# Performance work log

Hardware: AMD Instinct MI355X
Metric: run time of the kernel (lower is better)

The kernel has to match this reference:

```python
import jax, jax.numpy as jnp
import numpy as np

N = 100000   # nodes
E = 625000   # edges
D = 128      # input feature dim
H = 128      # hidden_channels
L = 2        # num_layers
NEG = 0.2    # leaky relu negative slope
BN_EPS = 1e-5


def setup_inputs() -> dict:
    key = jax.random.key(0)
    ks = jax.random.split(key, 12)
    s = 0.05
    return {
        "x": jax.random.normal(ks[0], (N, D), jnp.float32),
        "edge_index": jax.random.randint(ks[1], (2, E), 0, N, dtype=jnp.int32),
        "Wl": jax.random.normal(ks[2], (L, D, H), jnp.float32) * s,   # GATv2 lin_l (source)
        "bl": jax.random.normal(ks[3], (L, H), jnp.float32) * s,
        "Wr": jax.random.normal(ks[4], (L, D, H), jnp.float32) * s,   # GATv2 lin_r (target)
        "br": jax.random.normal(ks[5], (L, H), jnp.float32) * s,
        "att": jax.random.normal(ks[6], (L, H), jnp.float32) * s,     # attention vector a
        "cb": jax.random.normal(ks[7], (L, H), jnp.float32) * s,      # conv output bias
        "Wlin": jax.random.normal(ks[8], (L, H, H), jnp.float32) * s, # extra Linear
        "blin": jax.random.normal(ks[9], (L, H), jnp.float32) * s,
        "gamma": jnp.ones((L, H), jnp.float32),                       # BatchNorm weight
        "beta": jnp.zeros((L, H), jnp.float32),                       # BatchNorm bias
    }


def reference(x, edge_index, Wl, bl, Wr, br, att, cb, Wlin, blin, gamma, beta):
    src, dst = edge_index[0], edge_index[1]
    for i in range(L):
        # GATv2Conv (1 head, no self-loops)
        xs = x @ Wl[i] + bl[i]                 # [N, H] source transform
        xd = x @ Wr[i] + br[i]                 # [N, H] target transform
        e = jax.nn.leaky_relu(xs[src] + xd[dst], NEG)   # [E, H]
        logits = e @ att[i]                    # [E]
        m = jax.ops.segment_max(logits, dst, num_segments=N)
        a = jnp.exp(logits - m[dst])
        denom = jax.ops.segment_sum(a, dst, num_segments=N) + 1e-16
        alpha = a / denom[dst]                 # scatter-softmax over dst
        out = jax.ops.segment_sum(alpha[:, None] * xs[src], dst, num_segments=N) + cb[i]
        # x += lin(x)
        out = out + out @ Wlin[i] + blin[i]
        # BatchNorm1d (training mode: batch stats, biased var)
        mu = out.mean(axis=0)
        var = out.var(axis=0)
        x = (out - mu) * jax.lax.rsqrt(var + BN_EPS) * gamma[i] + beta[i]
        if i < L - 1:
            x = jax.nn.relu(x)
    return x
```

## Files before the change

### kernel.cpp

```cpp
#include <hip/hip_runtime.h>

#define NN 100000
#define NE 625000
#define HD 128

typedef unsigned int u32;
typedef unsigned short u16;
typedef __bf16 bf16x8 __attribute__((ext_vector_type(8)));
typedef float f32x4 __attribute__((ext_vector_type(4)));

__device__ __forceinline__ u16 f2b(float f) {
  u32 u = __float_as_uint(f);
  u32 r = (u + 0x7FFFu + ((u >> 16) & 1u)) >> 16;
  return (u16)r;
}
__device__ __forceinline__ float b2f(u32 u) { return __uint_as_float(u << 16); }

__global__ void k_prep_w(const float* __restrict__ Wl, const float* __restrict__ Wr,
                         const float* __restrict__ Wlin, u16* __restrict__ Wt) {
  int i = blockIdx.x * blockDim.x + threadIdx.x;
  if (i >= 6 * 16384) return;
  int mat = i >> 14;
  int l = mat / 3, which = mat % 3;
  int rem = i & 16383;
  int hh = rem >> 7, dd = rem & 127;
  const float* src = (which == 0) ? Wl : (which == 1) ? Wr : Wlin;
  float v = src[l * 16384 + dd * 128 + hh];
  if (which == 2 && dd == hh) v += 1.0f;
  Wt[l * (3 * 16384) + which * 16384 + hh * 128 + dd] = f2b(v);
}

__global__ void k_cast_x(const float* __restrict__ x, u16* __restrict__ xb) {
  int i = blockIdx.x * blockDim.x + threadIdx.x;
  if (i >= NN * 32) return;
  float4 v = *(const float4*)(x + i * 4);
  uint2 o;
  o.x = (u32)f2b(v.x) | ((u32)f2b(v.y) << 16);
  o.y = (u32)f2b(v.z) | ((u32)f2b(v.w) << 16);
  *(uint2*)(xb + i * 4) = o;
}

__global__ void k_hist(const int* __restrict__ dst, int* __restrict__ deg) {
  int e = blockIdx.x * blockDim.x + threadIdx.x;
  if (e < NE) atomicAdd(&deg[dst[e]], 1);
}

__global__ void k_alloc(const int* __restrict__ deg, int* __restrict__ row_start,
                        int* __restrict__ cursor) {
  int idx = blockIdx.x * blockDim.x + threadIdx.x;
  int lane = threadIdx.x & 63;
  int v = (idx < NN) ? deg[idx] : 0;
  int incl = v;
  #pragma unroll
  for (int off = 1; off < 64; off <<= 1) {
    int t = __shfl_up(incl, off, 64);
    if (lane >= off) incl += t;
  }
  int total = __shfl(incl, 63, 64);
  int base = 0;
  if (lane == 63) base = atomicAdd(cursor, total);
  base = __shfl(base, 63, 64);
  if (idx < NN) row_start[idx] = base + incl - v;
}

__global__ void k_fill(const int* __restrict__ src, const int* __restrict__ dst,
                       const int* __restrict__ row_start, int* __restrict__ cnt,
                       int* __restrict__ ss) {
  int e = blockIdx.x * blockDim.x + threadIdx.x;
  if (e >= NE) return;
  int d = dst[e];
  int p = row_start[d] + atomicAdd(&cnt[d], 1);
  ss[p] = src[e];
}

__global__ __launch_bounds__(256) void k_gemm_big(
    const u16* __restrict__ A, const u16* __restrict__ Bt0, const u16* __restrict__ Bt1,
    const float* __restrict__ bias0, const float* __restrict__ bias1,
    u16* __restrict__ o0, u16* __restrict__ o1,
    const float* __restrict__ bn_sum, const float* __restrict__ bn_sq,
    const float* __restrict__ bn_g, const float* __restrict__ bn_b,
    float* __restrict__ st_sum, float* __restrict__ st_sq, int nB) {
  __shared__ __align__(16) u16 lA[128 * 132];
  __shared__ __align__(16) u16 lB[128 * 128];
  const int tid = threadIdx.x;
  const int m0 = blockIdx.x * 128;
  const int rr = tid >> 4;
  const int seg = tid & 15;
  const int sK = seg >> 2;
  const int qd = seg & 3;

  float mu[8], sc[8], bb[8];
  if (bn_sum) {
    const float invn = 1.0f / 100000.0f;
    #pragma unroll
    for (int j = 0; j < 8; ++j) {
      int c = seg * 8 + j;
      float m = bn_sum[c] * invn;
      float v = fmaxf(bn_sq[c] * invn - m * m, 0.f);
      mu[j] = m;
      sc[j] = rsqrtf(v + 1e-5f) * bn_g[c];
      bb[j] = bn_b[c];
    }
  }
  #pragma unroll
  for (int p = 0; p < 8; ++p) {
    int g = m0 + p * 16 + rr;
    int gc = (g < NN) ? g : (NN - 1);
    uint4 v = *(const uint4*)(A + gc * HD + seg * 8);
    if (bn_sum) {
      u32 w[4] = {v.x, v.y, v.z, v.w};
      #pragma unroll
      for (int k = 0; k < 4; ++k) {
        float lo = fmaxf((b2f(w[k] & 0xFFFFu) - mu[2 * k]) * sc[2 * k] + bb[2 * k], 0.f);
        float hi = fmaxf((b2f(w[k] >> 16) - mu[2 * k + 1]) * sc[2 * k + 1] + bb[2 * k + 1], 0.f);
        w[k] = (u32)f2b(lo) | ((u32)f2b(hi) << 16);
      }
      v.x = w[0]; v.y = w[1]; v.z = w[2]; v.w = w[3];
    }
    *(uint4*)(lA + ((p * 4 + sK) * 64 + qd * 16 + rr) * 8) = v;
  }
  #pragma unroll
  for (int p = 0; p < 8; ++p) {
    int n = p * 16 + rr;
    uint4 v = *(const uint4*)(Bt0 + n * HD + seg * 8);
    *(uint4*)(lB + ((p * 4 + sK) * 64 + qd * 16 + rr) * 8) = v;
  }
  __syncthreads();

  const int wv = tid >> 6;
  const int lane = tid & 63;
  const int colt = lane & 15;
  const int rq = (lane >> 4) * 4;
  bf16x8 af[2][4];
  #pragma unroll
  for (int tile = 0; tile < 2; ++tile)
    #pragma unroll
    for (int s = 0; s < 4; ++s)
      af[tile][s] = *(const bf16x8*)(lA + (((wv * 2 + tile) * 4 + s) * 64 + lane) * 8);
  __syncthreads();

  for (int pass = 0; pass < nB; ++pass) {
    if (pass == 1) {
      __syncthreads();
      #pragma unroll
      for (int p = 0; p < 8; ++p) {
        int n = p * 16 + rr;
        uint4 v = *(const uint4*)(Bt1 + n * HD + seg * 8);
        *(uint4*)(lB + ((p * 4 + sK) * 64 + qd * 16 + rr) * 8) = v;
      }
      __syncthreads();
    }
    u16* o = (pass == 0) ? o0 : o1;
    const float* bias = (pass == 0) ? bias0 : bias1;
    #pragma unroll
    for (int t = 0; t < 8; ++t) {
      bf16x8 bf[4];
      #pragma unroll
      for (int s = 0; s < 4; ++s)
        bf[s] = *(const bf16x8*)(lB + ((t * 4 + s) * 64 + lane) * 8);
      const int c = t * 16 + colt;
      const float bs = bias[c];
      #pragma unroll
      for (int tile = 0; tile < 2; ++tile) {
        f32x4 acc = {0.f, 0.f, 0.f, 0.f};
        #pragma unroll
        for (int s = 0; s < 4; ++s)
          acc = __builtin_amdgcn_mfma_f32_16x16x32_bf16(af[tile][s], bf[s], acc, 0, 0, 0);
        #pragma unroll
        for (int r = 0; r < 4; ++r) {
          int lrow = (wv * 2 + tile) * 16 + rq + r;
          lA[lrow * 132 + c] = f2b(acc[r] + bs);
        }
      }
    }
    __syncthreads();
    float s8[8], q8[8];
    #pragma unroll
    for (int j = 0; j < 8; ++j) { s8[j] = 0.f; q8[j] = 0.f; }
    const int q = tid >> 4;
    #pragma unroll
    for (int i = 0; i < 8; ++i) {
      int row = i * 16 + q;
      int g = m0 + row;
      if (g < NN) {
        uint4 v = *(const uint4*)(lA + row * 132 + seg * 8);
        *(uint4*)(o + g * HD + seg * 8) = v;
        if (st_sum && pass == 0) {
          u32 w[4] = {v.x, v.y, v.z, v.w};
          #pragma unroll
          for (int k = 0; k < 4; ++k) {
            float lo = b2f(w[k] & 0xFFFFu), hi = b2f(w[k] >> 16);
            s8[2 * k] += lo; q8[2 * k] += lo * lo;
            s8[2 * k + 1] += hi; q8[2 * k + 1] += hi * hi;
          }
        }
      }
    }
    if (st_sum && pass == 0) {
      __syncthreads();
      float* red = (float*)lB;
      #pragma unroll
      for (int j = 0; j < 8; ++j) {
        red[q * 128 + seg * 8 + j] = s8[j];
        red[2048 + q * 128 + seg * 8 + j] = q8[j];
      }
      __syncthreads();
      if (tid < 128) {
        float S = 0.f, Q = 0.f;
        #pragma unroll
        for (int u = 0; u < 16; ++u) {
          S += red[u * 128 + tid];
          Q += red[2048 + u * 128 + tid];
        }
        atomicAdd(&st_sum[tid], S);
        atomicAdd(&st_sq[tid], Q);
      }
    }
  }
}

__global__ __launch_bounds__(256) void k_edge2(
    const u16* __restrict__ xs_b, const u16* __restrict__ xd_b,
    const int* __restrict__ row_start, const int* __restrict__ deg,
    const int* __restrict__ ss, const float* __restrict__ att,
    const float* __restrict__ cb, u16* __restrict__ out_b) {
  int dv = blockIdx.x * 4 + (threadIdx.x >> 6);
  if (dv >= NN) return;
  int lane = threadIdx.x & 63;
  float a0 = att[2 * lane], a1 = att[2 * lane + 1];
  const u32* xs32 = (const u32*)xs_b;
  u32 xdp = ((const u32*)xd_b)[dv * 64 + lane];
  float xd0 = b2f(xdp & 0xFFFFu), xd1 = b2f(xdp >> 16);
  int base = row_start[dv], n = deg[dv];
  float acc0 = 0.f, acc1 = 0.f, wsum = 0.f;
  int e = 0;
  for (; e + 4 <= n; e += 4) {
    int s0 = ss[base + e], s1 = ss[base + e + 1];
    int s2 = ss[base + e + 2], s3 = ss[base + e + 3];
    u32 p0 = xs32[s0 * 64 + lane];
    u32 p1 = xs32[s1 * 64 + lane];
    u32 p2 = xs32[s2 * 64 + lane];
    u32 p3 = xs32[s3 * 64 + lane];
    float x00 = b2f(p0 & 0xFFFFu), x01 = b2f(p0 >> 16);
    float x10 = b2f(p1 & 0xFFFFu), x11 = b2f(p1 >> 16);
    float x20 = b2f(p2 & 0xFFFFu), x21 = b2f(p2 >> 16);
    float x30 = b2f(p3 & 0xFFFFu), x31 = b2f(p3 >> 16);
    float t;
    float q0, q1, q2, q3;
    t = x00 + xd0; q0  = a0 * (fmaxf(t, 0.f) + 0.2f * fminf(t, 0.f));
    t = x01 + xd1; q0 += a1 * (fmaxf(t, 0.f) + 0.2f * fminf(t, 0.f));
    t = x10 + xd0; q1  = a0 * (fmaxf(t, 0.f) + 0.2f * fminf(t, 0.f));
    t = x11 + xd1; q1 += a1 * (fmaxf(t, 0.f) + 0.2f * fminf(t, 0.f));
    t = x20 + xd0; q2  = a0 * (fmaxf(t, 0.f) + 0.2f * fminf(t, 0.f));
    t = x21 + xd1; q2 += a1 * (fmaxf(t, 0.f) + 0.2f * fminf(t, 0.f));
    t = x30 + xd0; q3  = a0 * (fmaxf(t, 0.f) + 0.2f * fminf(t, 0.f));
    t = x31 + xd1; q3 += a1 * (fmaxf(t, 0.f) + 0.2f * fminf(t, 0.f));
    #pragma unroll
    for (int off = 1; off < 64; off <<= 1) {
      q0 += __shfl_xor(q0, off, 64);
      q1 += __shfl_xor(q1, off, 64);
      q2 += __shfl_xor(q2, off, 64);
      q3 += __shfl_xor(q3, off, 64);
    }
    float w0 = __expf(q0), w1 = __expf(q1), w2 = __expf(q2), w3 = __expf(q3);
    wsum += (w0 + w1) + (w2 + w3);
    acc0 += w0 * x00 + w1 * x10 + w2 * x20 + w3 * x30;
    acc1 += w0 * x01 + w1 * x11 + w2 * x21 + w3 * x31;
  }
  for (; e < n; ++e) {
    int s = ss[base + e];
    u32 p = xs32[s * 64 + lane];
    float x0 = b2f(p & 0xFFFFu), x1 = b2f(p >> 16);
    float t0 = x0 + xd0, t1 = x1 + xd1;
    float q = a0 * (fmaxf(t0, 0.f) + 0.2f * fminf(t0, 0.f)) +
              a1 * (fmaxf(t1, 0.f) + 0.2f * fminf(t1, 0.f));
    #pragma unroll
    for (int off = 1; off < 64; off <<= 1) q += __shfl_xor(q, off, 64);
    float w = __expf(q);
    wsum += w; acc0 += w * x0; acc1 += w * x1;
  }
  float inv = 1.f / (wsum + 1e-16f);
  float o0 = acc0 * inv + cb[2 * lane];
  float o1 = acc1 * inv + cb[2 * lane + 1];
  ((u32*)out_b)[dv * 64 + lane] = (u32)f2b(o0) | ((u32)f2b(o1) << 16);
}

__global__ void k_bn(const u16* __restrict__ hb, const float* __restrict__ ssum,
                     const float* __restrict__ ssq, const float* __restrict__ gamma,
                     const float* __restrict__ beta, float* __restrict__ fout) {
  int i = blockIdx.x * blockDim.x + threadIdx.x;
  if (i >= NN * 64) return;
  int cp = (i & 63) * 2;
  u32 xp = ((const u32*)hb)[i];
  float v0 = b2f(xp & 0xFFFFu), v1 = b2f(xp >> 16);
  const float invn = 1.0f / 100000.0f;
  float mu0 = ssum[cp] * invn, mu1 = ssum[cp + 1] * invn;
  float va0 = fmaxf(ssq[cp] * invn - mu0 * mu0, 0.f);
  float va1 = fmaxf(ssq[cp + 1] * invn - mu1 * mu1, 0.f);
  float s0 = rsqrtf(va0 + 1e-5f) * gamma[cp];
  float s1 = rsqrtf(va1 + 1e-5f) * gamma[cp + 1];
  float o0 = (v0 - mu0) * s0 + beta[cp];
  float o1 = (v1 - mu1) * s1 + beta[cp + 1];
  int row = i >> 6;
  *(float2*)(fout + row * 128 + cp) = make_float2(o0, o1);
}

extern "C" void kernel_launch(void* const* d_in, const int* in_sizes, int n_in,
                              void* d_out, int out_size, void* d_ws, size_t ws_size,
                              hipStream_t stream) {
  const float* x    = (const float*)d_in[0];
  const int*   ei   = (const int*)d_in[1];
  const float* Wl   = (const float*)d_in[2];
  const float* bl   = (const float*)d_in[3];
  const float* Wr   = (const float*)d_in[4];
  const float* br   = (const float*)d_in[5];
  const float* att  = (const float*)d_in[6];
  const float* cb   = (const float*)d_in[7];
  const float* Wlin = (const float*)d_in[8];
  const float* blin = (const float*)d_in[9];
  const float* gm   = (const float*)d_in[10];
  const float* bt   = (const float*)d_in[11];
  const int* esrc = ei;
  const int* edst = ei + NE;

  u16* xb    = (u16*)d_ws;
  u16* xs_b  = xb + NN * HD;
  u16* xd_b  = xs_b + NN * HD;
  u16* out_b = xd_b + NN * HD;
  u16* Wt    = out_b + NN * HD;
  int* deg       = (int*)(Wt + 6 * 16384);
  int* cnt       = deg + NN;
  int* cursor    = cnt + NN;
  int* row_start = cursor + 1;
  int* srcs      = row_start + NN;
  float* ssum0   = (float*)(srcs + NE);
  float* ssq0    = ssum0 + 128;
  float* ssum1   = ssq0 + 128;
  float* ssq1    = ssum1 + 128;

  hipMemsetAsync(deg, 0, (size_t)(2 * NN + 1) * 4, stream);
  hipMemsetAsync(ssum0, 0, 4 * 128 * 4, stream);
  k_prep_w<<<(6 * 16384 + 255) / 256, 256, 0, stream>>>(Wl, Wr, Wlin, Wt);
  k_cast_x<<<(NN * 32 + 255) / 256, 256, 0, stream>>>(x, xb);
  k_hist<<<(NE + 255) / 256, 256, 0, stream>>>(edst, deg);
  k_alloc<<<(NN + 255) / 256, 256, 0, stream>>>(deg, row_start, cursor);
  k_fill<<<(NE + 255) / 256, 256, 0, stream>>>(esrc, edst, row_start, cnt, srcs);

  const int gg = (NN + 127) / 128;
  const u16* wt0_l = Wt;             const u16* wt0_r = Wt + 16384;     const u16* wt0_lin = Wt + 2 * 16384;
  const u16* wt1_l = Wt + 3 * 16384; const u16* wt1_r = Wt + 4 * 16384; const u16* wt1_lin = Wt + 5 * 16384;

  k_gemm_big<<<gg, 256, 0, stream>>>(xb, wt0_l, wt0_r, bl, br, xs_b, xd_b,
                                     nullptr, nullptr, nullptr, nullptr,
                                     nullptr, nullptr, 2);
  k_edge2<<<(NN + 3) / 4, 256, 0, stream>>>(xs_b, xd_b, row_start, deg, srcs,
                                            att, cb, out_b);
  k_gemm_big<<<gg, 256, 0, stream>>>(out_b, wt0_lin, nullptr, blin, nullptr,
                                     out_b, nullptr,
                                     nullptr, nullptr, nullptr, nullptr,
                                     ssum0, ssq0, 1);
  k_gemm_big<<<gg, 256, 0, stream>>>(out_b, wt1_l, wt1_r, bl + 128, br + 128,
                                     xs_b, xd_b,
                                     ssum0, ssq0, gm, bt,
                                     nullptr, nullptr, 2);
  k_edge2<<<(NN + 3) / 4, 256, 0, stream>>>(xs_b, xd_b, row_start, deg, srcs,
                                            att + 128, cb + 128, out_b);
  k_gemm_big<<<gg, 256, 0, stream>>>(out_b, wt1_lin, nullptr, blin + 128, nullptr,
                                     out_b, nullptr,
                                     nullptr, nullptr, nullptr, nullptr,
                                     ssum1, ssq1, 1);
  k_bn<<<(NN * 64 + 255) / 256, 256, 0, stream>>>(out_b, ssum1, ssq1,
                                                  gm + 128, bt + 128, (float*)d_out);
}
```

Measured before the change: 484.3 us.

## Load GEMM weights from global memory and batch edge-logit reductions across four edges

The GEMM kernel no longer stages the weight matrix in LDS. Each lane reads its bf16x8 B fragments straight from global/L2, which halves shared memory per block and removes one staging phase and its barriers. The edge kernel now computes leaky ReLU as 0.6*t+0.4*|t| on packed float2. It folds four edge logits into one shared butterfly reduction (transpose-style combining at offsets 1 and 2, then a single chain) instead of four full chains, and handles the tail with masked weights rather than a scalar remainder loop. The risks are repeated global weight reads per block and wasted lanes on low-degree nodes.

```diff
diff --git a/kernel.cpp b/kernel.cpp
--- a/kernel.cpp
+++ b/kernel.cpp
@@ -8,6 +8,7 @@
 typedef unsigned short u16;
 typedef __bf16 bf16x8 __attribute__((ext_vector_type(8)));
 typedef float f32x4 __attribute__((ext_vector_type(4)));
+typedef float f32x2 __attribute__((ext_vector_type(2)));
 
 __device__ __forceinline__ u16 f2b(float f) {
   u32 u = __float_as_uint(f);
@@ -73,7 +74,7 @@
   ss[p] = src[e];
 }
 
-__global__ __launch_bounds__(256) void k_gemm_big(
+__global__ __launch_bounds__(256) void k_gemm3(
     const u16* __restrict__ A, const u16* __restrict__ Bt0, const u16* __restrict__ Bt1,
     const float* __restrict__ bias0, const float* __restrict__ bias1,
     u16* __restrict__ o0, u16* __restrict__ o1,
@@ -81,7 +82,6 @@
     const float* __restrict__ bn_g, const float* __restrict__ bn_b,
     float* __restrict__ st_sum, float* __restrict__ st_sq, int nB) {
   __shared__ __align__(16) u16 lA[128 * 132];
-  __shared__ __align__(16) u16 lB[128 * 128];
   const int tid = threadIdx.x;
   const int m0 = blockIdx.x * 128;
   const int rr = tid >> 4;
@@ -119,18 +119,13 @@
     }
     *(uint4*)(lA + ((p * 4 + sK) * 64 + qd * 16 + rr) * 8) = v;
   }
-  #pragma unroll
-  for (int p = 0; p < 8; ++p) {
-    int n = p * 16 + rr;
-    uint4 v = *(const uint4*)(Bt0 + n * HD + seg * 8);
-    *(uint4*)(lB + ((p * 4 + sK) * 64 + qd * 16 + rr) * 8) = v;
-  }
   __syncthreads();
 
   const int wv = tid >> 6;
   const int lane = tid & 63;
   const int colt = lane & 15;
-  const int rq = (lane >> 4) * 4;
+  const int rq4 = lane >> 4;
+  const int rq = rq4 * 4;
   bf16x8 af[2][4];
   #pragma unroll
   for (int tile = 0; tile < 2; ++tile)
@@ -140,16 +135,8 @@
   __syncthreads();
 
   for (int pass = 0; pass < nB; ++pass) {
-    if (pass == 1) {
-      __syncthreads();
-      #pragma unroll
-      for (int p = 0; p < 8; ++p) {
-        int n = p * 16 + rr;
-        uint4 v = *(const uint4*)(Bt1 + n * HD + seg * 8);
-        *(uint4*)(lB + ((p * 4 + sK) * 64 + qd * 16 + rr) * 8) = v;
-      }
-      __syncthreads();
-    }
+    if (pass == 1) __syncthreads();
+    const u16* Bt = (pass == 0) ? Bt0 : Bt1;
     u16* o = (pass == 0) ? o0 : o1;
     const float* bias = (pass == 0) ? bias0 : bias1;
     #pragma unroll
@@ -157,7 +144,7 @@
       bf16x8 bf[4];
       #pragma unroll
       for (int s = 0; s < 4; ++s)
-        bf[s] = *(const bf16x8*)(lB + ((t * 4 + s) * 64 + lane) * 8);
+        bf[s] = *(const bf16x8*)(Bt + (t * 16 + colt) * HD + s * 32 + rq4 * 8);
       const int c = t * 16 + colt;
       const float bs = bias[c];
       #pragma unroll
@@ -198,7 +185,7 @@
     }
     if (st_sum && pass == 0) {
       __syncthreads();
-      float* red = (float*)lB;
+      float* red = (float*)lA;
       #pragma unroll
       for (int j = 0; j < 8; ++j) {
         red[q * 128 + seg * 8 + j] = s8[j];
@@ -219,7 +206,7 @@
   }
 }
 
-__global__ __launch_bounds__(256) void k_edge2(
+__global__ __launch_bounds__(256) void k_edge3(
     const u16* __restrict__ xs_b, const u16* __restrict__ xd_b,
     const int* __restrict__ row_start, const int* __restrict__ deg,
     const int* __restrict__ ss, const float* __restrict__ att,
@@ -227,61 +214,68 @@
   int dv = blockIdx.x * 4 + (threadIdx.x >> 6);
   if (dv >= NN) return;
   int lane = threadIdx.x & 63;
-  float a0 = att[2 * lane], a1 = att[2 * lane + 1];
+  float2 av = *(const float2*)(att + 2 * lane);
+  f32x2 a6 = {0.6f * av.x, 0.6f * av.y};
+  f32x2 a4 = {0.4f * av.x, 0.4f * av.y};
+  u32 xdp = ((const u32*)xd_b)[dv * 64 + lane];
+  f32x2 xd2 = {b2f(xdp & 0xFFFFu), b2f(xdp >> 16)};
+  int base = row_start[dv], n = deg[dv];
   const u32* xs32 = (const u32*)xs_b;
-  u32 xdp = ((const u32*)xd_b)[dv * 64 + lane];
-  float xd0 = b2f(xdp & 0xFFFFu), xd1 = b2f(xdp >> 16);
-  int base = row_start[dv], n = deg[dv];
-  float acc0 = 0.f, acc1 = 0.f, wsum = 0.f;
-  int e = 0;
-  for (; e + 4 <= n; e += 4) {
-    int s0 = ss[base + e], s1 = ss[base + e + 1];
-    int s2 = ss[base + e + 2], s3 = ss[base + e + 3];
-    u32 p0 = xs32[s0 * 64 + lane];
-    u32 p1 = xs32[s1 * 64 + lane];
-    u32 p2 = xs32[s2 * 64 + lane];
-    u32 p3 = xs32[s3 * 64 + lane];
-    float x00 = b2f(p0 & 0xFFFFu), x01 = b2f(p0 >> 16);
-    float x10 = b2f(p1 & 0xFFFFu), x11 = b2f(p1 >> 16);
-    float x20 = b2f(p2 & 0xFFFFu), x21 = b2f(p2 >> 16);
-    float x30 = b2f(p3 & 0xFFFFu), x31 = b2f(p3 >> 16);
-    float t;
-    float q0, q1, q2, q3;
-    t = x00 + xd0; q0  = a0 * (fmaxf(t, 0.f) + 0.2f * fminf(t, 0.f));
-    t = x01 + xd1; q0 += a1 * (fmaxf(t, 0.f) + 0.2f * fminf(t, 0.f));
-    t = x10 + xd0; q1  = a0 * (fmaxf(t, 0.f) + 0.2f * fminf(t, 0.f));
-    t = x11 + xd1; q1 += a1 * (fmaxf(t, 0.f) + 0.2f * fminf(t, 0.f));
-    t = x20 + xd0; q2  = a0 * (fmaxf(t, 0.f) + 0.2f * fminf(t, 0.f));
-    t = x21 + xd1; q2 += a1 * (fmaxf(t, 0.f) + 0.2f * fminf(t, 0.f));
-    t = x30 + xd0; q3  = a0 * (fmaxf(t, 0.f) + 0.2f * fminf(t, 0.f));
-    t = x31 + xd1; q3 += a1 * (fmaxf(t, 0.f) + 0.2f * fminf(t, 0.f));
-    #pragma unroll
-    for (int off = 1; off < 64; off <<= 1) {
-      q0 += __shfl_xor(q0, off, 64);
-      q1 += __shfl_xor(q1, off, 64);
-      q2 += __shfl_xor(q2, off, 64);
-      q3 += __shfl_xor(q3, off, 64);
-    }
-    float w0 = __expf(q0), w1 = __expf(q1), w2 = __expf(q2), w3 = __expf(q3);
+  f32x2 acc = {0.f, 0.f};
+  float wsum = 0.f;
+  for (int e0 = 0; e0 < n; e0 += 4) {
+    int idx[4];
+    #pragma unroll
+    for (int j = 0; j < 4; ++j) {
+      int e = e0 + j;
+      idx[j] = ss[base + ((e < n) ? e : 0)];
+    }
+    f32x2 xv[4];
+    #pragma unroll
+    for (int j = 0; j < 4; ++j) {
+      u32 p = xs32[idx[j] * 64 + lane];
+      f32x2 t = {b2f(p & 0xFFFFu), b2f(p >> 16)};
+      xv[j] = t;
+    }
+    float q[4];
+    #pragma unroll
+    for (int j = 0; j < 4; ++j) {
+      f32x2 t = xv[j] + xd2;
+      f32x2 ab = {__builtin_fabsf(t.x), __builtin_fabsf(t.y)};
+      f32x2 qv = a4 * ab + a6 * t;
+      q[j] = qv.x + qv.y;
+    }
+    float sA0 = (lane & 1) ? q[1] : q[0];
+    float oA0 = (lane & 1) ? q[0] : q[1];
+    sA0 += __shfl_xor(oA0, 1, 64);
+    float sA1 = (lane & 1) ? q[3] : q[2];
+    float oA1 = (lane & 1) ? q[2] : q[3];
+    sA1 += __shfl_xor(oA1, 1, 64);
+    float sC = (lane & 2) ? sA1 : sA0;
+    float oC = (lane & 2) ? sA0 : sA1;
+    sC += __shfl_xor(oC, 2, 64);
+    sC += __shfl_xor(sC, 4, 64);
+    sC += __shfl_xor(sC, 8, 64);
+    sC += __shfl_xor(sC, 16, 64);
+    sC += __shfl_xor(sC, 32, 64);
+    float eE = __expf(sC);
+    float w0 = __shfl(eE, 0, 64);
+    float w1 = __shfl(eE, 1, 64);
+    float w2 = __shfl(eE, 2, 64);
+    float w3 = __shfl(eE, 3, 64);
+    w1 = (e0 + 1 < n) ? w1 : 0.f;
+    w2 = (e0 + 2 < n) ? w2 : 0.f;
+    w3 = (e0 + 3 < n) ? w3 : 0.f;
     wsum += (w0 + w1) + (w2 + w3);
-    acc0 += w0 * x00 + w1 * x10 + w2 * x20 + w3 * x30;
-    acc1 += w0 * x01 + w1 * x11 + w2 * x21 + w3 * x31;
-  }
-  for (; e < n; ++e) {
-    int s = ss[base + e];
-    u32 p = xs32[s * 64 + lane];
-    float x0 = b2f(p & 0xFFFFu), x1 = b2f(p >> 16);
-    float t0 = x0 + xd0, t1 = x1 + xd1;
-    float q = a0 * (fmaxf(t0, 0.f) + 0.2f * fminf(t0, 0.f)) +
-              a1 * (fmaxf(t1, 0.f) + 0.2f * fminf(t1, 0.f));
-    #pragma unroll
-    for (int off = 1; off < 64; off <<= 1) q += __shfl_xor(q, off, 64);
-    float w = __expf(q);
-    wsum += w; acc0 += w * x0; acc1 += w * x1;
+    acc += xv[0] * w0;
+    acc += xv[1] * w1;
+    acc += xv[2] * w2;
+    acc += xv[3] * w3;
   }
   float inv = 1.f / (wsum + 1e-16f);
-  float o0 = acc0 * inv + cb[2 * lane];
-  float o1 = acc1 * inv + cb[2 * lane + 1];
+  float2 cbv = *(const float2*)(cb + 2 * lane);
+  float o0 = acc.x * inv + cbv.x;
+  float o1 = acc.y * inv + cbv.y;
   ((u32*)out_b)[dv * 64 + lane] = (u32)f2b(o0) | ((u32)f2b(o1) << 16);
 }
 
@@ -350,25 +344,25 @@
   const u16* wt0_l = Wt;             const u16* wt0_r = Wt + 16384;     const u16* wt0_lin = Wt + 2 * 16384;
   const u16* wt1_l = Wt + 3 * 16384; const u16* wt1_r = Wt + 4 * 16384; const u16* wt1_lin = Wt + 5 * 16384;
 
-  k_gemm_big<<<gg, 256, 0, stream>>>(xb, wt0_l, wt0_r, bl, br, xs_b, xd_b,
-                                     nullptr, nullptr, nullptr, nullptr,
-                                     nullptr, nullptr, 2);
-  k_edge2<<<(NN + 3) / 4, 256, 0, stream>>>(xs_b, xd_b, row_start, deg, srcs,
+  k_gemm3<<<gg, 256, 0, stream>>>(xb, wt0_l, wt0_r, bl, br, xs_b, xd_b,
+                                  nullptr, nullptr, nullptr, nullptr,
+                                  nullptr, nullptr, 2);
+  k_edge3<<<(NN + 3) / 4, 256, 0, stream>>>(xs_b, xd_b, row_start, deg, srcs,
                                             att, cb, out_b);
-  k_gemm_big<<<gg, 256, 0, stream>>>(out_b, wt0_lin, nullptr, blin, nullptr,
-                                     out_b, nullptr,
-                                     nullptr, nullptr, nullptr, nullptr,
-                                     ssum0, ssq0, 1);
-  k_gemm_big<<<gg, 256, 0, stream>>>(out_b, wt1_l, wt1_r, bl + 128, br + 128,
-                                     xs_b, xd_b,
-                                     ssum0, ssq0, gm, bt,
-                                     nullptr, nullptr, 2);
-  k_edge2<<<(NN + 3) / 4, 256, 0, stream>>>(xs_b, xd_b, row_start, deg, srcs,
+  k_gemm3<<<gg, 256, 0, stream>>>(out_b, wt0_lin, nullptr, blin, nullptr,
+                                  out_b, nullptr,
+                                  nullptr, nullptr, nullptr, nullptr,
+                                  ssum0, ssq0, 1);
+  k_gemm3<<<gg, 256, 0, stream>>>(out_b, wt1_l, wt1_r, bl + 128, br + 128,
+                                  xs_b, xd_b,
+                                  ssum0, ssq0, gm, bt,
+                                  nullptr, nullptr, 2);
+  k_edge3<<<(NN + 3) / 4, 256, 0, stream>>>(xs_b, xd_b, row_start, deg, srcs,
                                             att + 128, cb + 128, out_b);
-  k_gemm_big<<<gg, 256, 0, stream>>>(out_b, wt1_lin, nullptr, blin + 128, nullptr,
-                                     out_b, nullptr,
-                                     nullptr, nullptr, nullptr, nullptr,
-                                     ssum1, ssq1, 1);
+  k_gemm3<<<gg, 256, 0, stream>>>(out_b, wt1_lin, nullptr, blin + 128, nullptr,
+                                  out_b, nullptr,
+                                  nullptr, nullptr, nullptr, nullptr,
+                                  ssum1, ssq1, 1);
   k_bn<<<(NN * 64 + 255) / 256, 256, 0, stream>>>(out_b, ssum1, ssq1,
                                                   gm + 128, bt + 128, (float*)d_out);
 }
```

After: 501.4 us. 1.04x slower.
